# Performance work log

Measured on AMD Instinct MI355X. Metric: run time of the kernel, lower is better.

Reference implementation:

```python
import jax, jax.numpy as jnp
import numpy as np

K = 3  # kernel size per spatial dim (stride=1, same padding)
MED_IDX = (K * K * K - 1) // 2  # torch.median returns the lower median; 27 taps -> index 13


def setup_inputs() -> dict:
    key = jax.random.key(0)
    x = jax.random.normal(key, (2, 1, 160, 160, 160), dtype=jnp.float32)
    return {"x": x}


def _median_pool3d(x):
    # same padding for k=3, stride=1: pad 1 (reflect) on each side of D, H, W
    xp = jnp.pad(x, ((0, 0), (0, 0), (1, 1), (1, 1), (1, 1)), mode="reflect")
    B, C, D, H, W = x.shape
    # gather the 27 shifted views (static slices; loop over fixed small kernel is fine)
    windows = [
        xp[:, :, i:i + D, j:j + H, l:l + W]
        for i in range(K) for j in range(K) for l in range(K)
    ]
    stack = jnp.stack(windows, axis=0)  # [27, B, C, D, H, W]
    # torch .median(dim=-1)[0] over 27 taps == sorted value at index 13
    return jnp.sort(stack, axis=0)[MED_IDX]


def reference(x):
    return _median_pool3d(x)
```

## Files before the change

### kernel.cpp

```cpp
#include <hip/hip_runtime.h>


typedef __fp16 hf2 __attribute__((ext_vector_type(2)));
typedef __fp16 hf4 __attribute__((ext_vector_type(4)));

#define DEV __device__ __forceinline__

DEV hf4 hmin4(hf4 a, hf4 b) { return __builtin_elementwise_min(a, b); }
DEV hf4 hmax4(hf4 a, hf4 b) { return __builtin_elementwise_max(a, b); }
DEV void ce(hf4& a, hf4& b) { hf4 lo = hmin4(a, b); hf4 hi = hmax4(a, b); a = lo; b = hi; }
DEV hf2 pk2(float a, float b) { return __builtin_amdgcn_cvt_pkrtz(a, b); }
DEV hf4 cat(hf2 a, hf2 b) { return __builtin_shufflevector(a, b, 0, 1, 2, 3); }

DEV void sort3(hf4& a, hf4& b, hf4& c) { ce(a, b); ce(a, c); ce(b, c); }

DEV void merge21(hf4 a0, hf4 a1, hf4 b0, hf4 z[3]) {
    hf4 e0 = a0, e1 = b0; ce(e0, e1);
    z[0] = e0; z[1] = a1; z[2] = e1; ce(z[1], z[2]);
}
DEV void merge22(hf4 a0, hf4 a1, hf4 b0, hf4 b1, hf4 z[4]) {
    hf4 p0 = a0, p1 = b0; ce(p0, p1);
    hf4 q0 = a1, q1 = b1; ce(q0, q1);
    z[0] = p0; z[1] = q0; z[2] = p1; ce(z[1], z[2]); z[3] = q1;
}
DEV void merge31(hf4 a0, hf4 a1, hf4 a2, hf4 b0, hf4 z[4]) {
    hf4 e[3]; merge21(a0, a2, b0, e);
    z[0] = e[0]; z[1] = a1; z[2] = e[1]; ce(z[1], z[2]); z[3] = e[2];
}
DEV void merge32(hf4 a0, hf4 a1, hf4 a2, hf4 b0, hf4 b1, hf4 z[5]) {
    hf4 e[3]; merge21(a0, a2, b0, e);
    hf4 o0 = a1, o1 = b1; ce(o0, o1);
    z[0] = e[0];
    z[1] = o0; z[2] = e[1]; ce(z[1], z[2]);
    z[3] = o1; z[4] = e[2]; ce(z[3], z[4]);
}
DEV void merge33(const hf4 a[3], const hf4 b[3], hf4 z[6]) {
    hf4 e[4]; merge22(a[0], a[2], b[0], b[2], e);
    hf4 o0 = a[1], o1 = b[1]; ce(o0, o1);
    z[0] = e[0];
    z[1] = o0; z[2] = e[1]; ce(z[1], z[2]);
    z[3] = o1; z[4] = e[2]; ce(z[3], z[4]);
    z[5] = e[3];
}
DEV void merge63(const hf4 a[6], const hf4 b[3], hf4 z[9]) {
    hf4 e[5]; merge32(a[0], a[2], a[4], b[0], b[2], e);
    hf4 o[4]; merge31(a[1], a[3], a[5], b[1], o);
    z[0] = e[0];
    z[1] = o[0]; z[2] = e[1]; ce(z[1], z[2]);
    z[3] = o[1]; z[4] = e[2]; ce(z[3], z[4]);
    z[5] = o[2]; z[6] = e[3]; ce(z[5], z[6]);
    z[7] = o[3]; z[8] = e[4]; ce(z[7], z[8]);
}
DEV void merge44(const hf4 a[4], const hf4 b[4], hf4 z[8]) {
    hf4 e[4]; merge22(a[0], a[2], b[0], b[2], e);
    hf4 o[4]; merge22(a[1], a[3], b[1], b[3], o);
    z[0] = e[0];
    z[1] = o[0]; z[2] = e[1]; ce(z[1], z[2]);
    z[3] = o[1]; z[4] = e[2]; ce(z[3], z[4]);
    z[5] = o[2]; z[6] = e[3]; ce(z[5], z[6]);
    z[7] = o[3];
}
DEV void merge55(const hf4 a[5], const hf4 b[5], hf4 z[10]) {
    hf4 ae[3] = {a[0], a[2], a[4]}, be[3] = {b[0], b[2], b[4]};
    hf4 e[6]; merge33(ae, be, e);
    hf4 o[4]; merge22(a[1], a[3], b[1], b[3], o);
    z[0] = e[0];
    z[1] = o[0]; z[2] = e[1]; ce(z[1], z[2]);
    z[3] = o[1]; z[4] = e[2]; ce(z[3], z[4]);
    z[5] = o[2]; z[6] = e[3]; ce(z[5], z[6]);
    z[7] = o[3]; z[8] = e[4]; ce(z[7], z[8]);
    z[9] = e[5];
}
DEV void merge99(const hf4 a[9], const hf4 b[9], hf4 z[18]) {
    hf4 ae[5] = {a[0], a[2], a[4], a[6], a[8]};
    hf4 be[5] = {b[0], b[2], b[4], b[6], b[8]};
    hf4 e[10]; merge55(ae, be, e);
    hf4 ao[4] = {a[1], a[3], a[5], a[7]};
    hf4 bo[4] = {b[1], b[3], b[5], b[7]};
    hf4 o[8]; merge44(ao, bo, o);
    z[0] = e[0];
#pragma unroll
    for (int i = 0; i < 8; i++) {
        z[2 * i + 1] = o[i];
        z[2 * i + 2] = e[i + 1];
        ce(z[2 * i + 1], z[2 * i + 2]);
    }
    z[17] = e[9];
}

DEV void sort_plane(const float* __restrict__ pb, const int ro[3], int cL, int x0, int cR,
                    hf4 M[9]) {
    hf4 r[3][3];
#pragma unroll
    for (int i = 0; i < 3; i++) {
        const float* p = pb + ro[i];
        float a = p[cL];
        float4 v = *reinterpret_cast<const float4*>(p + x0);
        float d = p[cR];
        hf2 pAL = pk2(a, v.x);
        hf2 pAC = pk2(v.x, v.y);
        hf2 pSH = pk2(v.y, v.z);
        hf2 pBC = pk2(v.z, v.w);
        hf2 pBR = pk2(v.w, d);
        r[i][0] = cat(pAL, pSH);
        r[i][1] = cat(pAC, pBC);
        r[i][2] = cat(pSH, pBR);
        sort3(r[i][0], r[i][1], r[i][2]);
    }
    hf4 s6[6]; merge33(r[0], r[1], s6);
    merge63(s6, r[2], M);
}

DEV hf4 sel13(const hf4 E[18], const hf4 R[9]) {
    hf4 m = E[13];
#pragma unroll
    for (int i = 0; i < 9; i++) m = hmin4(m, hmax4(R[i], E[12 - i]));
    return m;
}

constexpr int Bb = 2, Dd = 160, Hh = 160, Ww = 160;
constexpr int HW = Hh * Ww;
constexpr int WQ = Ww / 4;
constexpr int TPC = Hh * WQ;
constexpr int CH = 8;
constexpr int NCH = Dd / CH;
constexpr int TOTAL = Bb * NCH * TPC;

__global__ __launch_bounds__(256, 4) void MedianPool3d_68994354642979_kernel(
    const float* __restrict__ in, float* __restrict__ out) {
    int tid = blockIdx.x * 256 + threadIdx.x;
    int q = tid % WQ;
    int rest = tid / WQ;
    int y = rest % Hh;
    rest /= Hh;
    int chunk = rest % NCH;
    int b = rest / NCH;
    int x0 = q * 4;

    int ym = (y == 0) ? 1 : y - 1;
    int yp = (y == Hh - 1) ? Hh - 2 : y + 1;
    int ro[3] = {ym * Ww, y * Ww, yp * Ww};
    int cL = (x0 == 0) ? 1 : x0 - 1;
    int cR = (x0 + 4 == Ww) ? (Ww - 2) : x0 + 4;

    const float* base = in + (size_t)b * Dd * HW;
    float* ob = out + (size_t)b * Dd * HW;
    int z0 = chunk * CH;

    auto planeptr = [&](int p) {
        if (p < 0) p = -p;
        if (p >= Dd) p = 2 * Dd - 2 - p;
        return base + (size_t)p * HW;
    };

    hf4 SS[4][9];
    sort_plane(planeptr(z0 - 1), ro, cL, x0, cR, SS[0]);
    sort_plane(planeptr(z0),     ro, cL, x0, cR, SS[1]);
    sort_plane(planeptr(z0 + 1), ro, cL, x0, cR, SS[2]);

#pragma unroll
    for (int j = 0; j < CH / 2; j++) {
        const int z = z0 + 2 * j;
        const int sA = (2 * j) & 3;
        const int sB = (2 * j + 1) & 3;
        const int sC = (2 * j + 2) & 3;
        const int sD = (2 * j + 3) & 3;

        sort_plane(planeptr(z + 2), ro, cL, x0, cR, SS[sD]);

        hf4 E[18];
        merge99(SS[sB], SS[sC], E);
        hf4 m0 = sel13(E, SS[sA]);
        hf4 m1 = sel13(E, SS[sD]);

        float* o0 = ob + (size_t)z * HW + ro[1] + x0;
        float* o1 = o0 + HW;
        *reinterpret_cast<float4*>(o0) =
            make_float4((float)m0.x, (float)m0.y, (float)m0.z, (float)m0.w);
        *reinterpret_cast<float4*>(o1) =
            make_float4((float)m1.x, (float)m1.y, (float)m1.z, (float)m1.w);

        if (j < CH / 2 - 1)
            sort_plane(planeptr(z + 3), ro, cL, x0, cR, SS[sA]);
    }
}

extern "C" void kernel_launch(void* const* d_in, const int* in_sizes, int n_in,
                              void* d_out, int out_size, void* d_ws, size_t ws_size,
                              hipStream_t stream) {
    const float* x = (const float*)d_in[0];
    float* out = (float*)d_out;
    constexpr int threads = 256;
    constexpr int blocks = TOTAL / threads;
    MedianPool3d_68994354642979_kernel<<<blocks, threads, 0, stream>>>(x, out);
}
```

Baseline: 28.35 us.

## Stage input planes in LDS via async global_load_lds with multi-buffered pipeline

```diff
diff --git a/kernel.cpp b/kernel.cpp
--- a/kernel.cpp
+++ b/kernel.cpp
@@ -88,29 +88,6 @@
     z[17] = e[9];
 }
 
-DEV void sort_plane(const float* __restrict__ pb, const int ro[3], int cL, int x0, int cR,
-                    hf4 M[9]) {
-    hf4 r[3][3];
-#pragma unroll
-    for (int i = 0; i < 3; i++) {
-        const float* p = pb + ro[i];
-        float a = p[cL];
-        float4 v = *reinterpret_cast<const float4*>(p + x0);
-        float d = p[cR];
-        hf2 pAL = pk2(a, v.x);
-        hf2 pAC = pk2(v.x, v.y);
-        hf2 pSH = pk2(v.y, v.z);
-        hf2 pBC = pk2(v.z, v.w);
-        hf2 pBR = pk2(v.w, d);
-        r[i][0] = cat(pAL, pSH);
-        r[i][1] = cat(pAC, pBC);
-        r[i][2] = cat(pSH, pBR);
-        sort3(r[i][0], r[i][1], r[i][2]);
-    }
-    hf4 s6[6]; merge33(r[0], r[1], s6);
-    merge63(s6, r[2], M);
-}
-
 DEV hf4 sel13(const hf4 E[18], const hf4 R[9]) {
     hf4 m = E[13];
 #pragma unroll
@@ -120,43 +97,93 @@
 
 constexpr int Bb = 2, Dd = 160, Hh = 160, Ww = 160;
 constexpr int HW = Hh * Ww;
-constexpr int WQ = Ww / 4;
-constexpr int TPC = Hh * WQ;
 constexpr int CH = 8;
 constexpr int NCH = Dd / CH;
-constexpr int TOTAL = Bb * NCH * TPC;
-
-__global__ __launch_bounds__(256, 4) void MedianPool3d_68994354642979_kernel(
+constexpr int TX = 5, TY = 10;
+constexpr int BROWS = 18;
+constexpr int BCOLS = 40;
+constexpr int PLANE = BROWS * BCOLS;
+constexpr int NBUF = 6;
+constexpr int NBLK = Bb * NCH * TY * TX;
+
+typedef __attribute__((address_space(1))) const unsigned int gas_u32;
+typedef __attribute__((address_space(3))) unsigned int las_u32;
+
+__global__ __launch_bounds__(128, 2) void MedianPool3d_68994354642979_kernel(
     const float* __restrict__ in, float* __restrict__ out) {
-    int tid = blockIdx.x * 256 + threadIdx.x;
-    int q = tid % WQ;
-    int rest = tid / WQ;
-    int y = rest % Hh;
-    rest /= Hh;
-    int chunk = rest % NCH;
-    int b = rest / NCH;
-    int x0 = q * 4;
-
-    int ym = (y == 0) ? 1 : y - 1;
-    int yp = (y == Hh - 1) ? Hh - 2 : y + 1;
-    int ro[3] = {ym * Ww, y * Ww, yp * Ww};
-    int cL = (x0 == 0) ? 1 : x0 - 1;
-    int cR = (x0 + 4 == Ww) ? (Ww - 2) : x0 + 4;
+    __shared__ float lds[NBUF * PLANE];
+
+    const int tid = threadIdx.x;
+    int bid = blockIdx.x;
+    const int tx = bid % TX; bid /= TX;
+    const int ty = bid % TY; bid /= TY;
+    const int chunk = bid % NCH;
+    const int b = bid / NCH;
+
+    const int lq = tid & 7;
+    const int ly = tid >> 3;
+    const int y0 = ty * 16;
+    const int x0t = tx * 32;
+    const int z0 = chunk * CH;
 
     const float* base = in + (size_t)b * Dd * HW;
     float* ob = out + (size_t)b * Dd * HW;
-    int z0 = chunk * CH;
-
-    auto planeptr = [&](int p) {
-        if (p < 0) p = -p;
-        if (p >= Dd) p = 2 * Dd - 2 - p;
-        return base + (size_t)p * HW;
+
+    auto fill = [&](int br) {
+        int p = z0 - 1 + br;
+        p = (p < 0) ? -p : (p > Dd - 1 ? 2 * Dd - 2 - p : p);
+        const float* pp = base + (size_t)p * HW;
+        float* buf = &lds[(br % NBUF) * PLANE];
+#pragma unroll
+        for (int k = 0; k < 2; k++) {
+            int i = k * 128 + tid;
+            if (i < PLANE / 4) {
+                int r = i / 10, c4 = i % 10;
+                int gy = y0 - 1 + r;
+                gy = (gy < 0) ? 1 : (gy > Hh - 1 ? Hh - 2 : gy);
+                int gx = x0t - 4 + 4 * c4;
+                gx = (gx < 0) ? 0 : (gx > Ww - 4 ? Ww - 4 : gx);
+                const float* src = pp + gy * Ww + gx;
+                float* dst = buf + (size_t)(k * 128 + (tid & ~63)) * 4;
+                __builtin_amdgcn_global_load_lds((gas_u32*)src, (las_u32*)dst,
+                                                 16, 0, 0);
+            }
+        }
     };
 
+    const int lcol = (tx == 0 && lq == 0) ? 1 : 3 + 4 * lq;
+    const int rcol = (tx == TX - 1 && lq == 7) ? 34 : 8 + 4 * lq;
+    const int mco = 4 + 4 * lq;
+
+    auto sortp = [&](int br, hf4(&M)[9]) {
+        const float* buf = &lds[(br % NBUF) * PLANE];
+        hf4 r[3][3];
+#pragma unroll
+        for (int i = 0; i < 3; i++) {
+            const float* rp = buf + (ly + i) * BCOLS;
+            float4 v = *reinterpret_cast<const float4*>(rp + mco);
+            float a = rp[lcol], d = rp[rcol];
+            hf2 pAL = pk2(a, v.x);
+            hf2 pAC = pk2(v.x, v.y);
+            hf2 pSH = pk2(v.y, v.z);
+            hf2 pBC = pk2(v.z, v.w);
+            hf2 pBR = pk2(v.w, d);
+            r[i][0] = cat(pAL, pSH);
+            r[i][1] = cat(pAC, pBC);
+            r[i][2] = cat(pSH, pBR);
+            sort3(r[i][0], r[i][1], r[i][2]);
+        }
+        hf4 s6[6]; merge33(r[0], r[1], s6);
+        merge63(s6, r[2], M);
+    };
+
+    fill(0); fill(1); fill(2); fill(3); fill(4);
+    __syncthreads();
     hf4 SS[4][9];
-    sort_plane(planeptr(z0 - 1), ro, cL, x0, cR, SS[0]);
-    sort_plane(planeptr(z0),     ro, cL, x0, cR, SS[1]);
-    sort_plane(planeptr(z0 + 1), ro, cL, x0, cR, SS[2]);
+    sortp(0, SS[0]);
+    sortp(1, SS[1]);
+    sortp(2, SS[2]);
+    __syncthreads();
 
 #pragma unroll
     for (int j = 0; j < CH / 2; j++) {
@@ -166,22 +193,26 @@
         const int sC = (2 * j + 2) & 3;
         const int sD = (2 * j + 3) & 3;
 
-        sort_plane(planeptr(z + 2), ro, cL, x0, cR, SS[sD]);
+        if (2 * j + 5 <= CH + 1) fill(2 * j + 5);
+        if (2 * j + 6 <= CH + 1) fill(2 * j + 6);
+
+        sortp(2 * j + 3, SS[sD]);
 
         hf4 E[18];
         merge99(SS[sB], SS[sC], E);
         hf4 m0 = sel13(E, SS[sA]);
         hf4 m1 = sel13(E, SS[sD]);
 
-        float* o0 = ob + (size_t)z * HW + ro[1] + x0;
+        float* o0 = ob + (size_t)z * HW + (y0 + ly) * Ww + x0t + 4 * lq;
         float* o1 = o0 + HW;
         *reinterpret_cast<float4*>(o0) =
             make_float4((float)m0.x, (float)m0.y, (float)m0.z, (float)m0.w);
         *reinterpret_cast<float4*>(o1) =
             make_float4((float)m1.x, (float)m1.y, (float)m1.z, (float)m1.w);
 
-        if (j < CH / 2 - 1)
-            sort_plane(planeptr(z + 3), ro, cL, x0, cR, SS[sA]);
+        if (j < CH / 2 - 1) sortp(2 * j + 4, SS[sA]);
+
+        __syncthreads();
     }
 }
 
@@ -190,7 +221,5 @@
                               hipStream_t stream) {
     const float* x = (const float*)d_in[0];
     float* out = (float*)d_out;
-    constexpr int threads = 256;
-    constexpr int blocks = TOTAL / threads;
-    MedianPool3d_68994354642979_kernel<<<blocks, threads, 0, stream>>>(x, out);
-}
+    MedianPool3d_68994354642979_kernel<<<NBLK, 128, 0, stream>>>(x, out);
+}
```

Result: slower. 32.73 us (+15.4%).

## Software-pipeline plane loads two planes ahead with scheduling fences

Applied to the files above, without the earlier changes.

```diff
diff --git a/kernel.cpp b/kernel.cpp
--- a/kernel.cpp
+++ b/kernel.cpp
@@ -5,6 +5,7 @@
 typedef __fp16 hf4 __attribute__((ext_vector_type(4)));
 
 #define DEV __device__ __forceinline__
+#define SCHED_FENCE() __builtin_amdgcn_sched_barrier(0)
 
 DEV hf4 hmin4(hf4 a, hf4 b) { return __builtin_elementwise_min(a, b); }
 DEV hf4 hmax4(hf4 a, hf4 b) { return __builtin_elementwise_max(a, b); }
@@ -88,20 +89,29 @@
     z[17] = e[9];
 }
 
-DEV void sort_plane(const float* __restrict__ pb, const int ro[3], int cL, int x0, int cR,
-                    hf4 M[9]) {
-    hf4 r[3][3];
+DEV void load18(const float* __restrict__ pb, const int ro[3], int cL, int x0, int cR,
+                float R[18]) {
 #pragma unroll
     for (int i = 0; i < 3; i++) {
         const float* p = pb + ro[i];
-        float a = p[cL];
+        R[i * 6 + 0] = p[cL];
         float4 v = *reinterpret_cast<const float4*>(p + x0);
-        float d = p[cR];
-        hf2 pAL = pk2(a, v.x);
-        hf2 pAC = pk2(v.x, v.y);
-        hf2 pSH = pk2(v.y, v.z);
-        hf2 pBC = pk2(v.z, v.w);
-        hf2 pBR = pk2(v.w, d);
+        R[i * 6 + 1] = v.x; R[i * 6 + 2] = v.y;
+        R[i * 6 + 3] = v.z; R[i * 6 + 4] = v.w;
+        R[i * 6 + 5] = p[cR];
+    }
+}
+
+DEV void sortp(const float R[18], hf4 M[9]) {
+    hf4 r[3][3];
+#pragma unroll
+    for (int i = 0; i < 3; i++) {
+        const float* q = R + i * 6;
+        hf2 pAL = pk2(q[0], q[1]);
+        hf2 pAC = pk2(q[1], q[2]);
+        hf2 pSH = pk2(q[2], q[3]);
+        hf2 pBC = pk2(q[3], q[4]);
+        hf2 pBR = pk2(q[4], q[5]);
         r[i][0] = cat(pAL, pSH);
         r[i][1] = cat(pAC, pBC);
         r[i][2] = cat(pSH, pBR);
@@ -121,12 +131,11 @@
 constexpr int Bb = 2, Dd = 160, Hh = 160, Ww = 160;
 constexpr int HW = Hh * Ww;
 constexpr int WQ = Ww / 4;
-constexpr int TPC = Hh * WQ;
 constexpr int CH = 8;
 constexpr int NCH = Dd / CH;
-constexpr int TOTAL = Bb * NCH * TPC;
-
-__global__ __launch_bounds__(256, 4) void MedianPool3d_68994354642979_kernel(
+constexpr int TOTAL = Bb * NCH * Hh * WQ;
+
+__global__ __launch_bounds__(256, 2) void MedianPool3d_68994354642979_kernel(
     const float* __restrict__ in, float* __restrict__ out) {
     int tid = blockIdx.x * 256 + threadIdx.x;
     int q = tid % WQ;
@@ -154,9 +163,21 @@
     };
 
     hf4 SS[4][9];
-    sort_plane(planeptr(z0 - 1), ro, cL, x0, cR, SS[0]);
-    sort_plane(planeptr(z0),     ro, cL, x0, cR, SS[1]);
-    sort_plane(planeptr(z0 + 1), ro, cL, x0, cR, SS[2]);
+    float RT0[18], RT1[18];
+
+    {
+        float P0[18], P1[18];
+        load18(planeptr(z0 - 1), ro, cL, x0, cR, P0);
+        load18(planeptr(z0),     ro, cL, x0, cR, P1);
+        load18(planeptr(z0 + 1), ro, cL, x0, cR, RT1);
+        load18(planeptr(z0 + 2), ro, cL, x0, cR, RT0);
+        SCHED_FENCE();
+        sortp(P0, SS[0]);
+        sortp(P1, SS[1]);
+        sortp(RT1, SS[2]);
+        load18(planeptr(z0 + 3), ro, cL, x0, cR, RT1);
+        SCHED_FENCE();
+    }
 
 #pragma unroll
     for (int j = 0; j < CH / 2; j++) {
@@ -166,7 +187,10 @@
         const int sC = (2 * j + 2) & 3;
         const int sD = (2 * j + 3) & 3;
 
-        sort_plane(planeptr(z + 2), ro, cL, x0, cR, SS[sD]);
+        sortp(RT0, SS[sD]);
+        if (j <= 2)
+            load18(planeptr(z + 4), ro, cL, x0, cR, RT0);
+        SCHED_FENCE();
 
         hf4 E[18];
         merge99(SS[sB], SS[sC], E);
@@ -180,8 +204,11 @@
         *reinterpret_cast<float4*>(o1) =
             make_float4((float)m1.x, (float)m1.y, (float)m1.z, (float)m1.w);
 
-        if (j < CH / 2 - 1)
-            sort_plane(planeptr(z + 3), ro, cL, x0, cR, SS[sA]);
+        if (j <= 2)
+            sortp(RT1, SS[sA]);
+        if (j <= 1)
+            load18(planeptr(z + 5), ro, cL, x0, cR, RT1);
+        SCHED_FENCE();
     }
 }
 
```

Measured after the change: 27.47 us. 3.1% less time.

## Stage halo plane tiles in LDS via async global_load_lds ring buffer

Applied to the files above, without the earlier changes.

```diff
diff --git a/kernel.cpp b/kernel.cpp
--- a/kernel.cpp
+++ b/kernel.cpp
@@ -88,29 +88,6 @@
     z[17] = e[9];
 }
 
-DEV void sort_plane(const float* __restrict__ pb, const int ro[3], int cL, int x0, int cR,
-                    hf4 M[9]) {
-    hf4 r[3][3];
-#pragma unroll
-    for (int i = 0; i < 3; i++) {
-        const float* p = pb + ro[i];
-        float a = p[cL];
-        float4 v = *reinterpret_cast<const float4*>(p + x0);
-        float d = p[cR];
-        hf2 pAL = pk2(a, v.x);
-        hf2 pAC = pk2(v.x, v.y);
-        hf2 pSH = pk2(v.y, v.z);
-        hf2 pBC = pk2(v.z, v.w);
-        hf2 pBR = pk2(v.w, d);
-        r[i][0] = cat(pAL, pSH);
-        r[i][1] = cat(pAC, pBC);
-        r[i][2] = cat(pSH, pBR);
-        sort3(r[i][0], r[i][1], r[i][2]);
-    }
-    hf4 s6[6]; merge33(r[0], r[1], s6);
-    merge63(s6, r[2], M);
-}
-
 DEV hf4 sel13(const hf4 E[18], const hf4 R[9]) {
     hf4 m = E[13];
 #pragma unroll
@@ -120,68 +97,128 @@
 
 constexpr int Bb = 2, Dd = 160, Hh = 160, Ww = 160;
 constexpr int HW = Hh * Ww;
-constexpr int WQ = Ww / 4;
-constexpr int TPC = Hh * WQ;
-constexpr int CH = 8;
+constexpr int STRIP = 5;
+constexpr int NSTRIP = Hh / STRIP;
+constexpr int CH = 10;
 constexpr int NCH = Dd / CH;
-constexpr int TOTAL = Bb * NCH * TPC;
+constexpr int TROWS = STRIP + 2;
+constexpr int PLANEF = TROWS * Ww;
+constexpr int NRING = 6;
+constexpr int NBLK = Bb * NCH * NSTRIP;
+
+typedef __attribute__((address_space(1))) const unsigned int gas_u32;
+typedef __attribute__((address_space(3))) unsigned int las_u32;
+
+#define WAIT_BARRIER()                                               \
+    do {                                                             \
+        asm volatile("s_waitcnt vmcnt(2) lgkmcnt(0)" ::: "memory");  \
+        __builtin_amdgcn_sched_barrier(0);                           \
+        __builtin_amdgcn_s_barrier();                                \
+        __builtin_amdgcn_sched_barrier(0);                           \
+    } while (0)
 
 __global__ __launch_bounds__(256, 4) void MedianPool3d_68994354642979_kernel(
     const float* __restrict__ in, float* __restrict__ out) {
-    int tid = blockIdx.x * 256 + threadIdx.x;
-    int q = tid % WQ;
-    int rest = tid / WQ;
-    int y = rest % Hh;
-    rest /= Hh;
-    int chunk = rest % NCH;
-    int b = rest / NCH;
-    int x0 = q * 4;
-
-    int ym = (y == 0) ? 1 : y - 1;
-    int yp = (y == Hh - 1) ? Hh - 2 : y + 1;
-    int ro[3] = {ym * Ww, y * Ww, yp * Ww};
-    int cL = (x0 == 0) ? 1 : x0 - 1;
-    int cR = (x0 + 4 == Ww) ? (Ww - 2) : x0 + 4;
+    __shared__ float lds[NRING * PLANEF];
+
+    const int tid = threadIdx.x;
+    int bid = blockIdx.x;
+    const int ty = bid % NSTRIP; bid /= NSTRIP;
+    const int zc = bid % NCH;
+    const int b  = bid / NCH;
+    const int z0 = zc * CH;
+    const int y0 = ty * STRIP;
 
     const float* base = in + (size_t)b * Dd * HW;
     float* ob = out + (size_t)b * Dd * HW;
-    int z0 = chunk * CH;
-
-    auto planeptr = [&](int p) {
-        if (p < 0) p = -p;
-        if (p >= Dd) p = 2 * Dd - 2 - p;
-        return base + (size_t)p * HW;
+
+    auto fill = [&](int m) {
+        int p = z0 - 1 + m;
+        p = (p < 0) ? 1 : ((p > Dd - 1) ? Dd - 2 : p);
+        const float* pp = base + (size_t)p * HW;
+        float* ldsb = &lds[(m % NRING) * PLANEF];
+        {
+            int row = tid / 40, c4 = tid % 40;
+            int gy = y0 - 1 + row;
+            gy = (gy < 0) ? 1 : ((gy > Hh - 1) ? Hh - 2 : gy);
+            const float* src = pp + gy * Ww + c4 * 4;
+            float* dst = ldsb + (size_t)(tid & ~63) * 4;
+            __builtin_amdgcn_global_load_lds((gas_u32*)src, (las_u32*)dst, 16, 0, 0);
+        }
+        if (tid < 24) {
+            int c = 256 + tid;
+            int c4 = c % 40;
+            int gy = y0 + 5;
+            gy = (gy > Hh - 1) ? Hh - 2 : gy;
+            const float* src = pp + gy * Ww + c4 * 4;
+            float* dst = ldsb + 256 * 4;
+            __builtin_amdgcn_global_load_lds((gas_u32*)src, (las_u32*)dst, 16, 0, 0);
+        }
     };
 
+    const int q = tid % 40;
+    const int ly = tid / 40;
+    const int x0 = q * 4;
+    const int cLi = (q == 0) ? 1 : (x0 - 1);
+    const int cRi = (q == 39) ? (Ww - 2) : (x0 + 4);
+
+    auto sortp = [&](int m, hf4(&M)[9]) {
+        const float* tb = &lds[(m % NRING) * PLANEF];
+        hf4 r[3][3];
+#pragma unroll
+        for (int i = 0; i < 3; i++) {
+            const float* rp = tb + (ly + i) * Ww;
+            float4 v = *reinterpret_cast<const float4*>(rp + x0);
+            float a = rp[cLi], d = rp[cRi];
+            hf2 pAL = pk2(a, v.x);
+            hf2 pAC = pk2(v.x, v.y);
+            hf2 pSH = pk2(v.y, v.z);
+            hf2 pBC = pk2(v.z, v.w);
+            hf2 pBR = pk2(v.w, d);
+            r[i][0] = cat(pAL, pSH);
+            r[i][1] = cat(pAC, pBC);
+            r[i][2] = cat(pSH, pBR);
+            sort3(r[i][0], r[i][1], r[i][2]);
+        }
+        hf4 s6[6]; merge33(r[0], r[1], s6);
+        merge63(s6, r[2], M);
+    };
+
+    fill(0); fill(1);
+    fill(2); fill(3);
+    fill(4); fill(5);
+    WAIT_BARRIER();
+
     hf4 SS[4][9];
-    sort_plane(planeptr(z0 - 1), ro, cL, x0, cR, SS[0]);
-    sort_plane(planeptr(z0),     ro, cL, x0, cR, SS[1]);
-    sort_plane(planeptr(z0 + 1), ro, cL, x0, cR, SS[2]);
+    if (tid < 200) { sortp(0, SS[0]); sortp(1, SS[1]); }
 
 #pragma unroll
     for (int j = 0; j < CH / 2; j++) {
-        const int z = z0 + 2 * j;
-        const int sA = (2 * j) & 3;
-        const int sB = (2 * j + 1) & 3;
-        const int sC = (2 * j + 2) & 3;
-        const int sD = (2 * j + 3) & 3;
-
-        sort_plane(planeptr(z + 2), ro, cL, x0, cR, SS[sD]);
-
-        hf4 E[18];
-        merge99(SS[sB], SS[sC], E);
-        hf4 m0 = sel13(E, SS[sA]);
-        hf4 m1 = sel13(E, SS[sD]);
-
-        float* o0 = ob + (size_t)z * HW + ro[1] + x0;
-        float* o1 = o0 + HW;
-        *reinterpret_cast<float4*>(o0) =
-            make_float4((float)m0.x, (float)m0.y, (float)m0.z, (float)m0.w);
-        *reinterpret_cast<float4*>(o1) =
-            make_float4((float)m1.x, (float)m1.y, (float)m1.z, (float)m1.w);
-
-        if (j < CH / 2 - 1)
-            sort_plane(planeptr(z + 3), ro, cL, x0, cR, SS[sA]);
+        WAIT_BARRIER();
+
+        if (2 * j + 7 <= CH + 1) { fill(2 * j + 6); fill(2 * j + 7); }
+
+        if (tid < 200) {
+            const int sA = (2 * j) & 3;
+            const int sB = (2 * j + 1) & 3;
+            const int sC = (2 * j + 2) & 3;
+            const int sD = (2 * j + 3) & 3;
+            sortp(2 * j + 2, SS[sC]);
+            sortp(2 * j + 3, SS[sD]);
+
+            hf4 E[18];
+            merge99(SS[sB], SS[sC], E);
+            hf4 m0 = sel13(E, SS[sA]);
+            hf4 m1 = sel13(E, SS[sD]);
+
+            const int z = z0 + 2 * j;
+            float* o0 = ob + (size_t)z * HW + (y0 + ly) * Ww + x0;
+            float* o1 = o0 + HW;
+            *reinterpret_cast<float4*>(o0) =
+                make_float4((float)m0.x, (float)m0.y, (float)m0.z, (float)m0.w);
+            *reinterpret_cast<float4*>(o1) =
+                make_float4((float)m1.x, (float)m1.y, (float)m1.z, (float)m1.w);
+        }
     }
 }
 
@@ -190,7 +227,5 @@
                               hipStream_t stream) {
     const float* x = (const float*)d_in[0];
     float* out = (float*)d_out;
-    constexpr int threads = 256;
-    constexpr int blocks = TOTAL / threads;
-    MedianPool3d_68994354642979_kernel<<<blocks, threads, 0, stream>>>(x, out);
-}
+    MedianPool3d_68994354642979_kernel<<<NBLK, 256, 0, stream>>>(x, out);
+}
```

After: 30.74 us. 8.4% more time.
